# Optimization experiments

Hardware: AMD Instinct MI355X
Metric: run time of the kernel (lower is better)

The kernel has to match this reference:

```python
import jax, jax.numpy as jnp
import numpy as np

NUM_HEADS = 16
HEAD_DIM = 96          # dim=1536 / 16 heads
ROPE_HALF = HEAD_DIM // 2   # 48 rotary frequencies
FREQ_PER_AXIS = ROPE_HALF // 3  # 16 frequencies per 3D coordinate axis
ROPE_BASE = 10000.0


def _rope_sincos(coords):
    # coords: [B, T, 3] -> sin, cos: [B, T, ROPE_HALF]
    inv_freq = 1.0 / (ROPE_BASE ** (jnp.arange(FREQ_PER_AXIS, dtype=jnp.float32) / FREQ_PER_AXIS))
    # angles per axis: [B, T, 3, F] -> concat axes -> [B, T, 3*F]
    ang = coords[..., :, None] * inv_freq  # [B, T, 3, F]
    ang = ang.reshape(*coords.shape[:-1], ROPE_HALF)
    return jnp.sin(ang), jnp.cos(ang)


def _apply_rotary(x, sin, cos):
    # x: [B, H, T, D]; sin/cos: [B, T, D/2] broadcast over heads
    s = sin[:, None, :, :]
    c = cos[:, None, :, :]
    x1, x2 = x[..., :ROPE_HALF], x[..., ROPE_HALF:]
    return jnp.concatenate([x1 * c - x2 * s, x2 * c + x1 * s], axis=-1)


def setup_inputs() -> dict:
    key = jax.random.key(0)
    ks = jax.random.split(key, 8)
    B, Tq, Tk, D = 2, 1024, 2048, 1536
    std = 1.0 / np.sqrt(D)
    return {
        "x": jax.random.normal(ks[0], (B, Tq, D), jnp.float32),
        "memory": jax.random.normal(ks[1], (B, Tk, D), jnp.float32),
        "query_coords": jax.random.normal(ks[2], (B, Tq, 3), jnp.float32),
        "memory_coords": jax.random.normal(ks[3], (B, Tk, 3), jnp.float32),
        "Wq": jax.random.normal(ks[4], (D, D), jnp.float32) * std,
        "bq": jnp.zeros((D,), jnp.float32),
        "Wk": jax.random.normal(ks[5], (D, D), jnp.float32) * std,
        "bk": jnp.zeros((D,), jnp.float32),
        "Wv": jax.random.normal(ks[6], (D, D), jnp.float32) * std,
        "bv": jnp.zeros((D,), jnp.float32),
        "Wo": jax.random.normal(ks[7], (D, D), jnp.float32) * std,
        "bo": jnp.zeros((D,), jnp.float32),
    }


def reference(x, memory, query_coords, memory_coords, Wq, bq, Wk, bk, Wv, bv, Wo, bo):
    B, Tq, D = x.shape
    Tk = memory.shape[1]
    H, Hd = NUM_HEADS, HEAD_DIM

    # projections (nn.Linear: y = x @ W^T + b)
    q = (jnp.einsum('btd,ed->bte', x, Wq) + bq).reshape(B, Tq, H, Hd).transpose(0, 2, 1, 3)
    k = (jnp.einsum('btd,ed->bte', memory, Wk) + bk).reshape(B, Tk, H, Hd).transpose(0, 2, 1, 3)
    v = (jnp.einsum('btd,ed->bte', memory, Wv) + bv).reshape(B, Tk, H, Hd).transpose(0, 2, 1, 3)

    # 3D-coordinate RoPE (identity augmentation: shift=0, jitter=1, rescale=1)
    q_sin, q_cos = _rope_sincos(query_coords)
    k_sin, k_cos = _rope_sincos(memory_coords)
    q = _apply_rotary(q, q_sin, q_cos)
    k = _apply_rotary(k, k_sin, k_cos)

    # SDPA (standard scaling): softmax(q k^T / sqrt(Hd)) v
    scale = 1.0 / jnp.sqrt(jnp.asarray(Hd, jnp.float32))
    scores = jnp.einsum('bhqd,bhkd->bhqk', q, k) * scale
    attn = jax.nn.softmax(scores, axis=-1)
    out = jnp.einsum('bhqk,bhkd->bhqd', attn, v)  # [B, H, Tq, Hd]

    out = out.transpose(0, 2, 1, 3).reshape(B, Tq, D)
    return jnp.einsum('btd,ed->bte', out, Wo) + bo
```

## Files before the change

kernel.cpp:

```cpp
#include <hip/hip_runtime.h>
#include <math.h>

typedef _Float16 f16;
typedef __attribute__((ext_vector_type(4))) _Float16 f16x4;
typedef __attribute__((ext_vector_type(8))) _Float16 f16x8;
typedef __attribute__((ext_vector_type(4))) float f32x4;
typedef __attribute__((ext_vector_type(16))) float f32x16;

#define NB 2
#define NH 16
#define TQ 1024
#define TK 2048
#define DM 1536
#define HD 96
#define RH 48

__device__ __forceinline__ f32x4 mfma16(f16x8 a, f16x8 b, f32x4 c) {
    return __builtin_amdgcn_mfma_f32_16x16x32_f16(a, b, c, 0, 0, 0);
}

#define GLDS16(gptr, lptr) __builtin_amdgcn_global_load_lds( \
    (const __attribute__((address_space(1))) unsigned int*)(gptr), \
    (__attribute__((address_space(3))) unsigned int*)(lptr), 16, 0, 0)

__global__ void cvt_w4(const float4* __restrict__ W0, const float4* __restrict__ W1,
                       const float4* __restrict__ W2, const float4* __restrict__ W3,
                       f16x4* __restrict__ o0, f16x4* __restrict__ o1,
                       f16x4* __restrict__ o2, f16x4* __restrict__ o3, int n4) {
    int i = blockIdx.x * 256 + threadIdx.x;
    if (i >= n4) return;
    const float4* in = blockIdx.y == 0 ? W0 : blockIdx.y == 1 ? W1 : blockIdx.y == 2 ? W2 : W3;
    f16x4* out      = blockIdx.y == 0 ? o0 : blockIdx.y == 1 ? o1 : blockIdx.y == 2 ? o2 : o3;
    float4 v = in[i];
    f16x4 o;
    o[0] = (f16)v.x; o[1] = (f16)v.y; o[2] = (f16)v.z; o[3] = (f16)v.w;
    out[i] = o;
}

__global__ void cvt_xm(const float4* __restrict__ X, const float4* __restrict__ M,
                       f16x4* __restrict__ ox, f16x4* __restrict__ om, int nx4, int nm4) {
    int i = blockIdx.x * 256 + threadIdx.x;
    int n = blockIdx.y == 0 ? nx4 : nm4;
    if (i >= n) return;
    const float4* in = blockIdx.y == 0 ? X : M;
    f16x4* out = blockIdx.y == 0 ? ox : om;
    float4 v = in[i];
    f16x4 o;
    o[0] = (f16)v.x; o[1] = (f16)v.y; o[2] = (f16)v.z; o[3] = (f16)v.w;
    out[i] = o;
}

__global__ void rope_tab2(const float* __restrict__ cq, const float* __restrict__ cm,
                          float* __restrict__ sq, float* __restrict__ cqo,
                          float* __restrict__ sk, float* __restrict__ cko,
                          int nq, int nk) {
    int i = blockIdx.x * 256 + threadIdx.x;
    int n = blockIdx.y == 0 ? nq : nk;
    if (i >= n) return;
    const float* coords = blockIdx.y == 0 ? cq : cm;
    float* sinT = blockIdx.y == 0 ? sq : sk;
    float* cosT = blockIdx.y == 0 ? cqo : cko;
    int bt = i / 48, idx = i - bt * 48;
    int axis = idx >> 4, f = idx & 15;
    float inv = powf(10000.f, -(float)f * (1.f / 16.f));
    float ang = coords[bt * 3 + axis] * inv;
    sinT[i] = sinf(ang);
    cosT[i] = cosf(ang);
}

__global__ void rope_apply_k(f16* __restrict__ qk, const float* __restrict__ sinT,
                             const float* __restrict__ cosT, int T, int stride,
                             float scale, int n) {
    int i = blockIdx.x * 256 + threadIdx.x;
    if (i >= n) return;
    int p = i % 48;
    int rest = i / 48;
    int t = rest % T;
    int b = rest / (NH * T);
    long base = (long)rest * stride;
    float x1 = (float)qk[base + p];
    float x2 = (float)qk[base + p + RH];
    int ti = (b * T + t) * 48 + p;
    float s = sinT[ti], c = cosT[ti];
    qk[base + p]      = (f16)((x1 * c - x2 * s) * scale);
    qk[base + p + RH] = (f16)((x2 * c + x1 * s) * scale);
}

template <int CFG>
__global__ __launch_bounds__(CFG == 0 ? 512 : 256, CFG == 0 ? 1 : 2)
void gemmP(const f16* __restrict__ Aq, const f16* __restrict__ Akv,
           const f16* __restrict__ Wqp, const f16* __restrict__ Wkp, const f16* __restrict__ Wvp,
           const float* __restrict__ bqp, const float* __restrict__ bkp, const float* __restrict__ bvp,
           f16* __restrict__ outq, f16* __restrict__ outk, f16* __restrict__ outv,
           float* __restrict__ outo) {
    constexpr int BMx = CFG == 0 ? 256 : 128;
    constexpr int BNx = CFG == 0 ? 256 : 128;
    constexpr int TPB = CFG == 0 ? 512 : 256;
    constexpr int MI  = CFG == 0 ? 8 : 4;
    constexpr int NI  = 4;
    constexpr int ABUF = BMx * 64;
    constexpr int BUFSZ = (BMx + BNx) * 64;
    constexpr int NT = DM / 64;

    __shared__ f16 Buf[2][BUFSZ];

    const int tid = threadIdx.x, w = tid >> 6, lane = tid & 63;
    const int l15 = lane & 15, g = lane >> 4;

    int sel = 0, mt, nt;
    const f16* A; const f16* W; const float* bias;
    if constexpr (CFG == 0) {
        const int bid = blockIdx.x;
        const int wid = (bid & 7) * 30 + (bid >> 3);
        if (wid < 48)       { sel = 0; mt = wid / 6;        nt = wid - mt * 6;        A = Aq;  W = Wqp; bias = bqp; }
        else if (wid < 144) { sel = 1; int r = wid - 48;  mt = r / 6; nt = r - mt * 6; A = Akv; W = Wkp; bias = bkp; }
        else                { sel = 2; int r = wid - 144; mt = r / 6; nt = r - mt * 6; A = Akv; W = Wvp; bias = bvp; }
    } else {
        const int bid = blockIdx.x;
        const int wid = (bid & 7) * 24 + (bid >> 3);
        mt = wid / 12; nt = wid - mt * 12;
        A = Aq; W = Wqp; bias = bqp;
    }
    const int m0 = mt * BMx, n0 = nt * BNx;
    const int wm = (w & 1) * (MI * 16);
    const int wn = (w >> 1) * 64;

    int src[4];
#pragma unroll
    for (int r = 0; r < 4; r++) {
        int L = r * (TPB * 16) + tid * 16;
        int row = L >> 7, seg = (L >> 4) & 7;
        src[r] = row * DM + ((seg ^ (row & 7)) << 3);
    }
    const f16* Ag = A + (long)m0 * DM;
    const f16* Bg = W + (long)n0 * DM;

    int aoff[MI][2], boff[NI][2];
#pragma unroll
    for (int i = 0; i < MI; i++) {
        int row = wm + i * 16 + l15;
#pragma unroll
        for (int s = 0; s < 2; s++)
            aoff[i][s] = row * 64 + (((s * 4 + g) ^ (row & 7)) << 3);
    }
#pragma unroll
    for (int j = 0; j < NI; j++) {
        int row = wn + j * 16 + l15;
#pragma unroll
        for (int s = 0; s < 2; s++)
            boff[j][s] = ABUF + row * 64 + (((s * 4 + g) ^ (row & 7)) << 3);
    }

#define STG(bufp, kt) do { \
    _Pragma("unroll") for (int r_ = 0; r_ < 4; r_++) { \
        GLDS16(Ag + src[r_] + (kt) * 64, &Buf[bufp][r_ * (TPB * 8) + w * 512]); \
        GLDS16(Bg + src[r_] + (kt) * 64, &Buf[bufp][ABUF + r_ * (TPB * 8) + w * 512]); \
    } \
} while (0)

    f32x4 acc[MI][NI] = {};

#define COMPUTE(bufp) do { \
    f16x8 bf[NI][2]; \
    _Pragma("unroll") for (int j_ = 0; j_ < NI; j_++) \
        _Pragma("unroll") for (int s_ = 0; s_ < 2; s_++) \
            bf[j_][s_] = *(const f16x8*)&Buf[bufp][boff[j_][s_]]; \
    __builtin_amdgcn_s_setprio(1); \
    _Pragma("unroll") for (int i_ = 0; i_ < MI; i_++) { \
        f16x8 a0 = *(const f16x8*)&Buf[bufp][aoff[i_][0]]; \
        f16x8 a1 = *(const f16x8*)&Buf[bufp][aoff[i_][1]]; \
        _Pragma("unroll") for (int j_ = 0; j_ < NI; j_++) { \
            acc[i_][j_] = mfma16(a0, bf[j_][0], acc[i_][j_]); \
            acc[i_][j_] = mfma16(a1, bf[j_][1], acc[i_][j_]); \
        } \
    } \
    __builtin_amdgcn_s_setprio(0); \
} while (0)

    STG(0, 0);
#pragma unroll 1
    for (int t = 0; t < NT; t += 2) {
        STG(1, t + 1);
        asm volatile("s_waitcnt vmcnt(8)" ::: "memory");
        __builtin_amdgcn_s_barrier();
        __builtin_amdgcn_sched_barrier(0);
        COMPUTE(0);
        __builtin_amdgcn_sched_barrier(0);
        __builtin_amdgcn_s_barrier();
        if (t + 2 < NT) {
            STG(0, t + 2);
            asm volatile("s_waitcnt vmcnt(8)" ::: "memory");
        } else {
            asm volatile("s_waitcnt vmcnt(0)" ::: "memory");
        }
        __builtin_amdgcn_s_barrier();
        __builtin_amdgcn_sched_barrier(0);
        COMPUTE(1);
        __builtin_amdgcn_sched_barrier(0);
        __builtin_amdgcn_s_barrier();
    }
#undef STG
#undef COMPUTE

#pragma unroll
    for (int i = 0; i < MI; i++) {
#pragma unroll
        for (int j = 0; j < NI; j++) {
            const int n = n0 + wn + j * 16 + l15;
            const int mb = m0 + wm + i * 16 + g * 4;
            if constexpr (CFG == 1) {
#pragma unroll
                for (int r = 0; r < 4; r++)
                    outo[(long)(mb + r) * DM + n] = acc[i][j][r] + bias[n];
            } else {
                const int hh = n / HD, hd = n - hh * HD;
                if (sel == 0) {
#pragma unroll
                    for (int r = 0; r < 4; r++) {
                        int m = mb + r, bq = m >> 10, t = m & (TQ - 1);
                        outq[(((long)bq * NH + hh) * TQ + t) * 96 + hd] = (f16)(acc[i][j][r] + bias[n]);
                    }
                } else if (sel == 1) {
#pragma unroll
                    for (int r = 0; r < 4; r++) {
                        int m = mb + r, bq = m >> 11, t = m & (TK - 1);
                        outk[(((long)bq * NH + hh) * TK + t) * 128 + hd] = (f16)(acc[i][j][r] + bias[n]);
                    }
                } else {
                    int bq = mb >> 11, t = mb & (TK - 1);
                    f16x4 pk;
#pragma unroll
                    for (int r = 0; r < 4; r++) pk[r] = (f16)(acc[i][j][r] + bias[n]);
                    *(f16x4*)&outv[(((long)bq * NH + hh) * HD + hd) * TK + t] = pk;
                }
            }
        }
    }
}

__global__ __launch_bounds__(256, 2) void attn_fwd(
    const f16* __restrict__ Q, const f16* __restrict__ Kg,
    const f16* __restrict__ Vg, f16* __restrict__ O) {
    __shared__ f16 Kl[2][64 * 128];
    __shared__ f16 Vl[2][96 * 64];
    __shared__ f16 Pl[4][32 * 64];

    const int tid = threadIdx.x, w = tid >> 6, lane = tid & 63;
    const int q31 = lane & 31, hf = lane >> 5;
    const int half = w >> 1, u = w & 1;

    const int linear = blockIdx.x + (int)(gridDim.x * (blockIdx.y + gridDim.y * blockIdx.z));
    const int wid = (linear & 7) * 64 + (linear >> 3);
    const int qc = wid & 15, h = (wid >> 4) & 15, b = wid >> 8;

    const long kbase = (long)(b * NH + h) * TK * 128;
    const long vbase = (long)(b * NH + h) * HD * TK;
    const long qbase = (long)(b * NH + h) * TQ * 96;
    const int q0 = qc * 64 + u * 32;

    int ksrc[8], vsrc[6];
#pragma unroll
    for (int i = 0; i < 8; i++) {
        int L = (u * 8 + i) * 1024 + lane * 16;
        int r = L >> 8, s = (L >> 4) & 15;
        ksrc[i] = r * 128 + ((s ^ (r & 7)) << 3);
    }
#pragma unroll
    for (int i = 0; i < 6; i++) {
        int L = (u * 6 + i) * 1024 + lane * 16;
        int r = L >> 7, s = (L >> 4) & 7;
        vsrc[i] = r * TK + ((s ^ (r & 7)) << 3);
    }

    f16x8 qf[6];
#pragma unroll
    for (int s = 0; s < 6; s++)
        qf[s] = *(const f16x8*)&Q[qbase + (long)(q0 + q31) * 96 + hf * 8 + 16 * s];

    float mx = -3e38f, ls = 0.f;
    f32x16 acc[3] = {};

#define STAGE(c_) do { \
    const f16* kp_ = Kg + kbase + (long)(half * 16 + (c_)) * (64 * 128); \
    _Pragma("unroll") for (int i_ = 0; i_ < 8; i_++) \
        GLDS16(kp_ + ksrc[i_], &Kl[half][(u * 8 + i_) * 512]); \
    const f16* vp_ = Vg + vbase + (half * 16 + (c_)) * 64; \
    _Pragma("unroll") for (int i_ = 0; i_ < 6; i_++) \
        GLDS16(vp_ + vsrc[i_], &Vl[half][(u * 6 + i_) * 512]); \
} while (0)

    STAGE(0);

    for (int c = 0; c < 16; ++c) {
        __syncthreads();

        f32x16 st[2] = {};
#pragma unroll
        for (int kt = 0; kt < 2; kt++)
#pragma unroll
            for (int s = 0; s < 6; s++) {
                f16x8 kf = *(const f16x8*)&Kl[half][(kt * 32 + q31) * 128 +
                                                    (((hf + 2 * s) ^ (q31 & 7)) << 3)];
                st[kt] = __builtin_amdgcn_mfma_f32_32x32x16_f16(kf, qf[s], st[kt], 0, 0, 0);
            }

        float t16[16];
#pragma unroll
        for (int r = 0; r < 16; r++) t16[r] = fmaxf(st[0][r], st[1][r]);
#pragma unroll
        for (int o = 8; o >= 1; o >>= 1)
#pragma unroll
            for (int r = 0; r < o; r++) t16[r] = fmaxf(t16[r], t16[r + o]);
        float cm = fmaxf(t16[0], __shfl_xor(t16[0], 32));
        float mn = fmaxf(mx, cm);
        float corr = exp2f(mx - mn);
        mx = mn;
#pragma unroll
        for (int kt = 0; kt < 2; kt++)
#pragma unroll
            for (int r = 0; r < 16; r++) st[kt][r] = exp2f(st[kt][r] - mn);
        float s16[16];
#pragma unroll
        for (int r = 0; r < 16; r++) s16[r] = st[0][r] + st[1][r];
#pragma unroll
        for (int o = 8; o >= 1; o >>= 1)
#pragma unroll
            for (int r = 0; r < o; r++) s16[r] += s16[r + o];
        ls = ls * corr + s16[0];
#pragma unroll
        for (int dt = 0; dt < 3; dt++)
#pragma unroll
            for (int r = 0; r < 16; r++) acc[dt][r] *= corr;

#pragma unroll
        for (int kt = 0; kt < 2; kt++)
#pragma unroll
            for (int jq = 0; jq < 4; jq++) {
                f16x4 pk;
#pragma unroll
                for (int e = 0; e < 4; e++) pk[e] = (f16)st[kt][jq * 4 + e];
                int seg = kt * 4 + jq;
                *(f16x4*)&Pl[w][q31 * 64 + ((seg ^ (q31 & 7)) << 3) + hf * 4] = pk;
            }

#pragma unroll
        for (int ks = 0; ks < 4; ks++) {
            f16x8 pf = *(const f16x8*)&Pl[w][q31 * 64 + (((hf + 2 * ks) ^ (q31 & 7)) << 3)];
#pragma unroll
            for (int dt = 0; dt < 3; dt++) {
                f16x8 vf = *(const f16x8*)&Vl[half][(dt * 32 + q31) * 64 +
                                                    (((hf + 2 * ks) ^ (q31 & 7)) << 3)];
                acc[dt] = __builtin_amdgcn_mfma_f32_32x32x16_f16(vf, pf, acc[dt], 0, 0, 0);
            }
        }

        __syncthreads();
        if (c < 15) STAGE(c + 1);
    }

    ls += __shfl_xor(ls, 32);
    float* dump = (float*)&Kl[0][0] + u * (64 * 52);
    __syncthreads();
    if (half == 1) {
        float* dl = dump + lane * 52;
        dl[0] = mx; dl[1] = ls;
#pragma unroll
        for (int dt = 0; dt < 3; dt++)
#pragma unroll
            for (int r = 0; r < 16; r++) dl[2 + dt * 16 + r] = acc[dt][r];
    }
    __syncthreads();
    if (half == 0) {
        const float* dl = dump + lane * 52;
        float mb = dl[0], lsb = dl[1];
        float mf = fmaxf(mx, mb);
        float ca = exp2f(mx - mf), cb = exp2f(mb - mf);
        float inv = 1.f / (ls * ca + lsb * cb);
        const long orow = (long)(b * TQ + q0 + q31) * DM + h * 96;
#pragma unroll
        for (int dt = 0; dt < 3; dt++)
#pragma unroll
            for (int jq = 0; jq < 4; jq++) {
                f16x4 ov;
#pragma unroll
                for (int e = 0; e < 4; e++) {
                    int r = jq * 4 + e;
                    ov[e] = (f16)((acc[dt][r] * ca + dl[2 + dt * 16 + r] * cb) * inv);
                }
                *(f16x4*)&O[orow + dt * 32 + jq * 8 + hf * 4] = ov;
            }
    }
}

extern "C" void kernel_launch(void* const* d_in, const int* in_sizes, int n_in,
                              void* d_out, int out_size, void* d_ws, size_t ws_size,
                              hipStream_t stream) {
    const float* x   = (const float*)d_in[0];
    const float* mem = (const float*)d_in[1];
    const float* qc  = (const float*)d_in[2];
    const float* mc  = (const float*)d_in[3];
    const float* Wq  = (const float*)d_in[4];
    const float* bq  = (const float*)d_in[5];
    const float* Wk  = (const float*)d_in[6];
    const float* bk  = (const float*)d_in[7];
    const float* Wv  = (const float*)d_in[8];
    const float* bv  = (const float*)d_in[9];
    const float* Wo  = (const float*)d_in[10];
    const float* bo  = (const float*)d_in[11];
    float* out = (float*)d_out;

    const long nx  = (long)NB * TQ * DM;
    const long nm  = (long)NB * TK * DM;
    const long nw  = (long)DM * DM;
    const long nq  = (long)NB * NH * TQ * 96;
    const long nkp = (long)NB * NH * TK * 128;
    const long nvt = (long)NB * NH * HD * TK;

    char* ws = (char*)d_ws;
    size_t off = 0;
    auto alloc = [&](size_t bytes) { size_t o = off; off = (off + bytes + 255) & ~(size_t)255; return o; };
    f16* x16   = (f16*)(ws + alloc(nx * 2));
    f16* mem16 = (f16*)(ws + alloc(nm * 2));
    f16* wq16  = (f16*)(ws + alloc(nw * 2));
    f16* wk16  = (f16*)(ws + alloc(nw * 2));
    f16* wv16  = (f16*)(ws + alloc(nw * 2));
    f16* wo16  = (f16*)(ws + alloc(nw * 2));
    f16* q16   = (f16*)(ws + alloc(nq * 2));
    f16* k16p  = (f16*)(ws + alloc(nkp * 2));
    f16* vt16  = (f16*)(ws + alloc(nvt * 2));
    float* sinq = (float*)(ws + alloc((size_t)NB * TQ * 48 * 4));
    float* cosq = (float*)(ws + alloc((size_t)NB * TQ * 48 * 4));
    float* sink = (float*)(ws + alloc((size_t)NB * TK * 48 * 4));
    float* cosk = (float*)(ws + alloc((size_t)NB * TK * 48 * 4));
    f16* at16 = x16;

    cvt_w4<<<dim3((int)(nw / 4 / 256), 4), 256, 0, stream>>>(
        (const float4*)Wq, (const float4*)Wk, (const float4*)Wv, (const float4*)Wo,
        (f16x4*)wq16, (f16x4*)wk16, (f16x4*)wv16, (f16x4*)wo16, (int)(nw / 4));
    cvt_xm<<<dim3((int)(nm / 4 / 256), 2), 256, 0, stream>>>(
        (const float4*)x, (const float4*)mem, (f16x4*)x16, (f16x4*)mem16,
        (int)(nx / 4), (int)(nm / 4));

    rope_tab2<<<dim3((NB * TK * 48 + 255) / 256, 2), 256, 0, stream>>>(
        qc, mc, sinq, cosq, sink, cosk, NB * TQ * 48, NB * TK * 48);

    gemmP<0><<<240, 512, 0, stream>>>(
        x16, mem16, wq16, wk16, wv16, bq, bk, bv, q16, k16p, vt16, nullptr);

    const float qscale = 0.10206207261596577f * 1.4426950408889634f;
    rope_apply_k<<<(NB * NH * TQ * 48 + 255) / 256, 256, 0, stream>>>(
        q16, sinq, cosq, TQ, 96, qscale, NB * NH * TQ * 48);
    rope_apply_k<<<(NB * NH * TK * 48 + 255) / 256, 256, 0, stream>>>(
        k16p, sink, cosk, TK, 128, 1.0f, NB * NH * TK * 48);

    attn_fwd<<<dim3(16, 16, 2), 256, 0, stream>>>(q16, k16p, vt16, at16);

    gemmP<1><<<192, 256, 0, stream>>>(
        at16, nullptr, wo16, nullptr, nullptr, bo, nullptr, nullptr,
        nullptr, nullptr, nullptr, out);
}
```

Measured before the change: 158.7 us.

## Split GEMM k-step into four quadrant phases to cut registers and allow two blocks

Replaces the per-k-tile compute, which loaded all B fragments and then streamed A, with four quadrant phases. Each phase loads only half the A or B fragments and issues its MFMAs between barriers, ping-ponging the fragments. This lowers live fragment registers so the 512-thread projection GEMM can target two blocks per CU, and it adds intra-iteration barriers for wave interleaving. The risks are extra barrier synchronisation, possible register spills under the tighter bound, and an LDS budget that may not fit two blocks.

After: 160.2 us. Within noise of the previous version (+1.0%).

```diff
diff --git a/kernel.cpp b/kernel.cpp
--- a/kernel.cpp
+++ b/kernel.cpp
@@ -87,7 +87,7 @@
 }
 
 template <int CFG>
-__global__ __launch_bounds__(CFG == 0 ? 512 : 256, CFG == 0 ? 1 : 2)
+__global__ __launch_bounds__(CFG == 0 ? 512 : 256, 2)
 void gemmP(const f16* __restrict__ Aq, const f16* __restrict__ Akv,
            const f16* __restrict__ Wqp, const f16* __restrict__ Wkp, const f16* __restrict__ Wvp,
            const float* __restrict__ bqp, const float* __restrict__ bkp, const float* __restrict__ bvp,
@@ -98,6 +98,7 @@
     constexpr int TPB = CFG == 0 ? 512 : 256;
     constexpr int MI  = CFG == 0 ? 8 : 4;
     constexpr int NI  = 4;
+    constexpr int MH  = MI / 2;
     constexpr int ABUF = BMx * 64;
     constexpr int BUFSZ = (BMx + BNx) * 64;
     constexpr int NT = DM / 64;
@@ -160,47 +161,84 @@
 
     f32x4 acc[MI][NI] = {};
 
-#define COMPUTE(bufp) do { \
-    f16x8 bf[NI][2]; \
-    _Pragma("unroll") for (int j_ = 0; j_ < NI; j_++) \
-        _Pragma("unroll") for (int s_ = 0; s_ < 2; s_++) \
-            bf[j_][s_] = *(const f16x8*)&Buf[bufp][boff[j_][s_]]; \
-    __builtin_amdgcn_s_setprio(1); \
-    _Pragma("unroll") for (int i_ = 0; i_ < MI; i_++) { \
-        f16x8 a0 = *(const f16x8*)&Buf[bufp][aoff[i_][0]]; \
-        f16x8 a1 = *(const f16x8*)&Buf[bufp][aoff[i_][1]]; \
-        _Pragma("unroll") for (int j_ = 0; j_ < NI; j_++) { \
-            acc[i_][j_] = mfma16(a0, bf[j_][0], acc[i_][j_]); \
-            acc[i_][j_] = mfma16(a1, bf[j_][1], acc[i_][j_]); \
-        } \
-    } \
-    __builtin_amdgcn_s_setprio(0); \
-} while (0)
-
     STG(0, 0);
 #pragma unroll 1
-    for (int t = 0; t < NT; t += 2) {
-        STG(1, t + 1);
-        asm volatile("s_waitcnt vmcnt(8)" ::: "memory");
-        __builtin_amdgcn_s_barrier();
-        __builtin_amdgcn_sched_barrier(0);
-        COMPUTE(0);
-        __builtin_amdgcn_sched_barrier(0);
-        __builtin_amdgcn_s_barrier();
-        if (t + 2 < NT) {
-            STG(0, t + 2);
+    for (int t = 0; t < NT; ++t) {
+        const int bi = t & 1;
+        if (t + 1 < NT) {
+            STG(bi ^ 1, t + 1);
             asm volatile("s_waitcnt vmcnt(8)" ::: "memory");
         } else {
             asm volatile("s_waitcnt vmcnt(0)" ::: "memory");
         }
         __builtin_amdgcn_s_barrier();
         __builtin_amdgcn_sched_barrier(0);
-        COMPUTE(1);
-        __builtin_amdgcn_sched_barrier(0);
+        const f16* bp = &Buf[bi][0];
+
+        f16x8 af[MH][2], bfL[2][2], bfH[2][2];
+#pragma unroll
+        for (int i = 0; i < MH; i++)
+#pragma unroll
+            for (int s = 0; s < 2; s++) af[i][s] = *(const f16x8*)&bp[aoff[i][s]];
+#pragma unroll
+        for (int j = 0; j < 2; j++)
+#pragma unroll
+            for (int s = 0; s < 2; s++) bfL[j][s] = *(const f16x8*)&bp[boff[j][s]];
+        __builtin_amdgcn_sched_barrier(0);
+        __builtin_amdgcn_s_setprio(1);
+#pragma unroll
+        for (int i = 0; i < MH; i++)
+#pragma unroll
+            for (int j = 0; j < 2; j++)
+#pragma unroll
+                for (int s = 0; s < 2; s++)
+                    acc[i][j] = mfma16(af[i][s], bfL[j][s], acc[i][j]);
+        __builtin_amdgcn_s_setprio(0);
         __builtin_amdgcn_s_barrier();
+        __builtin_amdgcn_sched_barrier(0);
+#pragma unroll
+        for (int j = 0; j < 2; j++)
+#pragma unroll
+            for (int s = 0; s < 2; s++) bfH[j][s] = *(const f16x8*)&bp[boff[2 + j][s]];
+        __builtin_amdgcn_sched_barrier(0);
+        __builtin_amdgcn_s_setprio(1);
+#pragma unroll
+        for (int i = 0; i < MH; i++)
+#pragma unroll
+            for (int j = 0; j < 2; j++)
+#pragma unroll
+                for (int s = 0; s < 2; s++)
+                    acc[i][2 + j] = mfma16(af[i][s], bfH[j][s], acc[i][2 + j]);
+        __builtin_amdgcn_s_setprio(0);
+        __builtin_amdgcn_s_barrier();
+        __builtin_amdgcn_sched_barrier(0);
+#pragma unroll
+        for (int i = 0; i < MH; i++)
+#pragma unroll
+            for (int s = 0; s < 2; s++) af[i][s] = *(const f16x8*)&bp[aoff[MH + i][s]];
+        __builtin_amdgcn_sched_barrier(0);
+        __builtin_amdgcn_s_setprio(1);
+#pragma unroll
+        for (int i = 0; i < MH; i++)
+#pragma unroll
+            for (int j = 0; j < 2; j++)
+#pragma unroll
+                for (int s = 0; s < 2; s++)
+                    acc[MH + i][2 + j] = mfma16(af[i][s], bfH[j][s], acc[MH + i][2 + j]);
+        __builtin_amdgcn_s_setprio(0);
+        __builtin_amdgcn_s_barrier();
+        __builtin_amdgcn_sched_barrier(0);
+        __builtin_amdgcn_s_setprio(1);
+#pragma unroll
+        for (int i = 0; i < MH; i++)
+#pragma unroll
+            for (int j = 0; j < 2; j++)
+#pragma unroll
+                for (int s = 0; s < 2; s++)
+                    acc[MH + i][j] = mfma16(af[i][s], bfL[j][s], acc[MH + i][j]);
+        __builtin_amdgcn_s_setprio(0);
     }
 #undef STG
-#undef COMPUTE
 
 #pragma unroll
     for (int i = 0; i < MI; i++) {
```

## Switch projection GEMM to 32x32x16 MFMA with software-pipelined LDS reads

Applied to the files above, without the earlier changes.

Rewrites the projection GEMM inner loop to use 32x32x16 MFMA tiles instead of 16x16x32, which halves the fragment loads per FLOP. LDS fragment reads for the next k-slice are interleaved with the MFMAs of the current one, and the main loop now processes one k-tile per iteration with a single double-buffer swap. It also raises the minimum-blocks hint for the 512-thread config to 2, which pressures registers. The aim is higher MFMA throughput and fewer LDS reads, at the cost of larger accumulators that might spill.

New measurement: 164.9 us, median of 2. +3.9%, slower.

```diff
diff --git a/kernel.cpp b/kernel.cpp
--- a/kernel.cpp
+++ b/kernel.cpp
@@ -87,7 +87,7 @@
 }
 
 template <int CFG>
-__global__ __launch_bounds__(CFG == 0 ? 512 : 256, CFG == 0 ? 1 : 2)
+__global__ __launch_bounds__(CFG == 0 ? 512 : 256, 2)
 void gemmP(const f16* __restrict__ Aq, const f16* __restrict__ Akv,
            const f16* __restrict__ Wqp, const f16* __restrict__ Wkp, const f16* __restrict__ Wvp,
            const float* __restrict__ bqp, const float* __restrict__ bkp, const float* __restrict__ bvp,
@@ -96,8 +96,7 @@
     constexpr int BMx = CFG == 0 ? 256 : 128;
     constexpr int BNx = CFG == 0 ? 256 : 128;
     constexpr int TPB = CFG == 0 ? 512 : 256;
-    constexpr int MI  = CFG == 0 ? 8 : 4;
-    constexpr int NI  = 4;
+    constexpr int MT  = CFG == 0 ? 4 : 2;
     constexpr int ABUF = BMx * 64;
     constexpr int BUFSZ = (BMx + BNx) * 64;
     constexpr int NT = DM / 64;
@@ -105,7 +104,7 @@
     __shared__ f16 Buf[2][BUFSZ];
 
     const int tid = threadIdx.x, w = tid >> 6, lane = tid & 63;
-    const int l15 = lane & 15, g = lane >> 4;
+    const int q31 = lane & 31, hf = lane >> 5;
 
     int sel = 0, mt, nt;
     const f16* A; const f16* W; const float* bias;
@@ -122,7 +121,7 @@
         A = Aq; W = Wqp; bias = bqp;
     }
     const int m0 = mt * BMx, n0 = nt * BNx;
-    const int wm = (w & 1) * (MI * 16);
+    const int wm = (w & 1) * (MT * 32);
     const int wn = (w >> 1) * 64;
 
     int src[4];
@@ -135,20 +134,20 @@
     const f16* Ag = A + (long)m0 * DM;
     const f16* Bg = W + (long)n0 * DM;
 
-    int aoff[MI][2], boff[NI][2];
-#pragma unroll
-    for (int i = 0; i < MI; i++) {
-        int row = wm + i * 16 + l15;
-#pragma unroll
-        for (int s = 0; s < 2; s++)
-            aoff[i][s] = row * 64 + (((s * 4 + g) ^ (row & 7)) << 3);
-    }
-#pragma unroll
-    for (int j = 0; j < NI; j++) {
-        int row = wn + j * 16 + l15;
-#pragma unroll
-        for (int s = 0; s < 2; s++)
-            boff[j][s] = ABUF + row * 64 + (((s * 4 + g) ^ (row & 7)) << 3);
+    int aoff[MT][4], boff[2][4];
+#pragma unroll
+    for (int i = 0; i < MT; i++) {
+        int row = wm + i * 32 + q31;
+#pragma unroll
+        for (int ks = 0; ks < 4; ks++)
+            aoff[i][ks] = row * 64 + (((ks * 2 + hf) ^ (row & 7)) << 3);
+    }
+#pragma unroll
+    for (int j = 0; j < 2; j++) {
+        int row = wn + j * 32 + q31;
+#pragma unroll
+        for (int ks = 0; ks < 4; ks++)
+            boff[j][ks] = ABUF + row * 64 + (((ks * 2 + hf) ^ (row & 7)) << 3);
     }
 
 #define STG(bufp, kt) do { \
@@ -158,80 +157,92 @@
     } \
 } while (0)
 
-    f32x4 acc[MI][NI] = {};
-
-#define COMPUTE(bufp) do { \
-    f16x8 bf[NI][2]; \
-    _Pragma("unroll") for (int j_ = 0; j_ < NI; j_++) \
-        _Pragma("unroll") for (int s_ = 0; s_ < 2; s_++) \
-            bf[j_][s_] = *(const f16x8*)&Buf[bufp][boff[j_][s_]]; \
+#define RD(aset, bset, ks) do { \
+    _Pragma("unroll") for (int i_ = 0; i_ < MT; i_++) \
+        aset[i_] = *(const f16x8*)&bp[aoff[i_][ks]]; \
+    _Pragma("unroll") for (int j_ = 0; j_ < 2; j_++) \
+        bset[j_] = *(const f16x8*)&bp[boff[j_][ks]]; \
+} while (0)
+
+#define MM(aset, bset) do { \
     __builtin_amdgcn_s_setprio(1); \
-    _Pragma("unroll") for (int i_ = 0; i_ < MI; i_++) { \
-        f16x8 a0 = *(const f16x8*)&Buf[bufp][aoff[i_][0]]; \
-        f16x8 a1 = *(const f16x8*)&Buf[bufp][aoff[i_][1]]; \
-        _Pragma("unroll") for (int j_ = 0; j_ < NI; j_++) { \
-            acc[i_][j_] = mfma16(a0, bf[j_][0], acc[i_][j_]); \
-            acc[i_][j_] = mfma16(a1, bf[j_][1], acc[i_][j_]); \
-        } \
-    } \
+    _Pragma("unroll") for (int i_ = 0; i_ < MT; i_++) \
+        _Pragma("unroll") for (int j_ = 0; j_ < 2; j_++) \
+            acc[i_][j_] = __builtin_amdgcn_mfma_f32_32x32x16_f16(aset[i_], bset[j_], acc[i_][j_], 0, 0, 0); \
     __builtin_amdgcn_s_setprio(0); \
 } while (0)
 
+    f32x16 acc[MT][2] = {};
+
     STG(0, 0);
 #pragma unroll 1
-    for (int t = 0; t < NT; t += 2) {
-        STG(1, t + 1);
-        asm volatile("s_waitcnt vmcnt(8)" ::: "memory");
-        __builtin_amdgcn_s_barrier();
-        __builtin_amdgcn_sched_barrier(0);
-        COMPUTE(0);
-        __builtin_amdgcn_sched_barrier(0);
-        __builtin_amdgcn_s_barrier();
-        if (t + 2 < NT) {
-            STG(0, t + 2);
+    for (int t = 0; t < NT; ++t) {
+        const int bi = t & 1;
+        if (t + 1 < NT) {
+            STG(bi ^ 1, t + 1);
             asm volatile("s_waitcnt vmcnt(8)" ::: "memory");
         } else {
             asm volatile("s_waitcnt vmcnt(0)" ::: "memory");
         }
         __builtin_amdgcn_s_barrier();
         __builtin_amdgcn_sched_barrier(0);
-        COMPUTE(1);
+        const f16* bp = &Buf[bi][0];
+
+        f16x8 fa0[MT], fb0[2], fa1[MT], fb1[2];
+        RD(fa0, fb0, 0);
+        RD(fa1, fb1, 1);
+        MM(fa0, fb0);
+        RD(fa0, fb0, 2);
+        MM(fa1, fb1);
+        RD(fa1, fb1, 3);
+        MM(fa0, fb0);
+        asm volatile("s_waitcnt lgkmcnt(0)" ::: "memory");
         __builtin_amdgcn_sched_barrier(0);
         __builtin_amdgcn_s_barrier();
+        MM(fa1, fb1);
     }
 #undef STG
-#undef COMPUTE
-
-#pragma unroll
-    for (int i = 0; i < MI; i++) {
-#pragma unroll
-        for (int j = 0; j < NI; j++) {
-            const int n = n0 + wn + j * 16 + l15;
-            const int mb = m0 + wm + i * 16 + g * 4;
+#undef RD
+#undef MM
+
+#pragma unroll
+    for (int i = 0; i < MT; i++) {
+#pragma unroll
+        for (int j = 0; j < 2; j++) {
+            const int n = n0 + wn + j * 32 + q31;
+            const float bn = bias[n];
             if constexpr (CFG == 1) {
 #pragma unroll
-                for (int r = 0; r < 4; r++)
-                    outo[(long)(mb + r) * DM + n] = acc[i][j][r] + bias[n];
+                for (int r = 0; r < 16; r++) {
+                    int m = m0 + wm + i * 32 + (r & 3) + 8 * (r >> 2) + 4 * hf;
+                    outo[(long)m * DM + n] = acc[i][j][r] + bn;
+                }
             } else {
                 const int hh = n / HD, hd = n - hh * HD;
                 if (sel == 0) {
 #pragma unroll
-                    for (int r = 0; r < 4; r++) {
-                        int m = mb + r, bq = m >> 10, t = m & (TQ - 1);
-                        outq[(((long)bq * NH + hh) * TQ + t) * 96 + hd] = (f16)(acc[i][j][r] + bias[n]);
+                    for (int r = 0; r < 16; r++) {
+                        int m = m0 + wm + i * 32 + (r & 3) + 8 * (r >> 2) + 4 * hf;
+                        int bq = m >> 10, t = m & (TQ - 1);
+                        outq[(((long)bq * NH + hh) * TQ + t) * 96 + hd] = (f16)(acc[i][j][r] + bn);
                     }
                 } else if (sel == 1) {
 #pragma unroll
-                    for (int r = 0; r < 4; r++) {
-                        int m = mb + r, bq = m >> 11, t = m & (TK - 1);
-                        outk[(((long)bq * NH + hh) * TK + t) * 128 + hd] = (f16)(acc[i][j][r] + bias[n]);
+                    for (int r = 0; r < 16; r++) {
+                        int m = m0 + wm + i * 32 + (r & 3) + 8 * (r >> 2) + 4 * hf;
+                        int bq = m >> 11, t = m & (TK - 1);
+                        outk[(((long)bq * NH + hh) * TK + t) * 128 + hd] = (f16)(acc[i][j][r] + bn);
                     }
                 } else {
-                    int bq = mb >> 11, t = mb & (TK - 1);
-                    f16x4 pk;
-#pragma unroll
-                    for (int r = 0; r < 4; r++) pk[r] = (f16)(acc[i][j][r] + bias[n]);
-                    *(f16x4*)&outv[(((long)bq * NH + hh) * HD + hd) * TK + t] = pk;
+#pragma unroll
+                    for (int g = 0; g < 4; g++) {
+                        int mb = m0 + wm + i * 32 + 8 * g + 4 * hf;
+                        int bq = mb >> 11, t = mb & (TK - 1);
+                        f16x4 pk;
+#pragma unroll
+                        for (int e = 0; e < 4; e++) pk[e] = (f16)(acc[i][j][4 * g + e] + bn);
+                        *(f16x4*)&outv[(((long)bq * NH + hh) * HD + hd) * TK + t] = pk;
+                    }
                 }
             }
         }
```

## Fuse Q rotary into attention, vectorize K rotary, merge conversion kernels

Applied to the files above, without the earlier changes.

Three changes. Q-side RoPE and softmax scaling now run inside the attention kernel on the Q fragments right after they are loaded, so the separate Q rope pass over global memory goes away. The K rope kernel is rewritten to handle 4 elements per thread with vector loads. The weight and activation fp32-to-fp16 conversions are merged into one launch. Together these cut kernel launches and memory traffic, at the cost of extra sin/cos loads in attention and idle blocks in the merged conversion grid, which is sized for the largest tensor.

Result: no change. 155.8 us (-1.8%).

```diff
diff --git a/kernel.cpp b/kernel.cpp
--- a/kernel.cpp
+++ b/kernel.cpp
@@ -23,27 +23,19 @@
     (const __attribute__((address_space(1))) unsigned int*)(gptr), \
     (__attribute__((address_space(3))) unsigned int*)(lptr), 16, 0, 0)
 
-__global__ void cvt_w4(const float4* __restrict__ W0, const float4* __restrict__ W1,
-                       const float4* __restrict__ W2, const float4* __restrict__ W3,
-                       f16x4* __restrict__ o0, f16x4* __restrict__ o1,
-                       f16x4* __restrict__ o2, f16x4* __restrict__ o3, int n4) {
+__global__ void cvt6(const float4* __restrict__ Wq, const float4* __restrict__ Wk,
+                     const float4* __restrict__ Wv, const float4* __restrict__ Wo,
+                     const float4* __restrict__ X,  const float4* __restrict__ M,
+                     f16x4* __restrict__ oq, f16x4* __restrict__ ok,
+                     f16x4* __restrict__ ov, f16x4* __restrict__ oo,
+                     f16x4* __restrict__ ox, f16x4* __restrict__ om,
+                     int nw4, int nx4, int nm4) {
     int i = blockIdx.x * 256 + threadIdx.x;
-    if (i >= n4) return;
-    const float4* in = blockIdx.y == 0 ? W0 : blockIdx.y == 1 ? W1 : blockIdx.y == 2 ? W2 : W3;
-    f16x4* out      = blockIdx.y == 0 ? o0 : blockIdx.y == 1 ? o1 : blockIdx.y == 2 ? o2 : o3;
-    float4 v = in[i];
-    f16x4 o;
-    o[0] = (f16)v.x; o[1] = (f16)v.y; o[2] = (f16)v.z; o[3] = (f16)v.w;
-    out[i] = o;
-}
-
-__global__ void cvt_xm(const float4* __restrict__ X, const float4* __restrict__ M,
-                       f16x4* __restrict__ ox, f16x4* __restrict__ om, int nx4, int nm4) {
-    int i = blockIdx.x * 256 + threadIdx.x;
-    int n = blockIdx.y == 0 ? nx4 : nm4;
+    const int y = blockIdx.y;
+    const int n = (y < 4) ? nw4 : (y == 4 ? nx4 : nm4);
     if (i >= n) return;
-    const float4* in = blockIdx.y == 0 ? X : M;
-    f16x4* out = blockIdx.y == 0 ? ox : om;
+    const float4* in = y == 0 ? Wq : y == 1 ? Wk : y == 2 ? Wv : y == 3 ? Wo : y == 4 ? X : M;
+    f16x4* out      = y == 0 ? oq : y == 1 ? ok : y == 2 ? ov : y == 3 ? oo : y == 4 ? ox : om;
     float4 v = in[i];
     f16x4 o;
     o[0] = (f16)v.x; o[1] = (f16)v.y; o[2] = (f16)v.z; o[3] = (f16)v.w;
@@ -68,22 +60,29 @@
     cosT[i] = cosf(ang);
 }
 
-__global__ void rope_apply_k(f16* __restrict__ qk, const float* __restrict__ sinT,
-                             const float* __restrict__ cosT, int T, int stride,
-                             float scale, int n) {
+__global__ void ropek4(f16* __restrict__ qk, const float* __restrict__ sinT,
+                       const float* __restrict__ cosT, int n) {
     int i = blockIdx.x * 256 + threadIdx.x;
     if (i >= n) return;
-    int p = i % 48;
-    int rest = i / 48;
-    int t = rest % T;
-    int b = rest / (NH * T);
-    long base = (long)rest * stride;
-    float x1 = (float)qk[base + p];
-    float x2 = (float)qk[base + p + RH];
-    int ti = (b * T + t) * 48 + p;
-    float s = sinT[ti], c = cosT[ti];
-    qk[base + p]      = (f16)((x1 * c - x2 * s) * scale);
-    qk[base + p + RH] = (f16)((x2 * c + x1 * s) * scale);
+    int j = i % 12, row = i / 12;
+    int p0 = j * 4;
+    int t = row & (TK - 1);
+    int b = row / (NH * TK);
+    long base = (long)row * 128;
+    float4 sv = *(const float4*)&sinT[((long)b * TK + t) * 48 + p0];
+    float4 cv = *(const float4*)&cosT[((long)b * TK + t) * 48 + p0];
+    f16x4 x1 = *(const f16x4*)&qk[base + p0];
+    f16x4 x2 = *(const f16x4*)&qk[base + p0 + RH];
+    f16x4 o1, o2;
+    float s[4] = {sv.x, sv.y, sv.z, sv.w}, c[4] = {cv.x, cv.y, cv.z, cv.w};
+#pragma unroll
+    for (int e = 0; e < 4; e++) {
+        float a = (float)x1[e], bb = (float)x2[e];
+        o1[e] = (f16)(a * c[e] - bb * s[e]);
+        o2[e] = (f16)(bb * c[e] + a * s[e]);
+    }
+    *(f16x4*)&qk[base + p0] = o1;
+    *(f16x4*)&qk[base + p0 + RH] = o2;
 }
 
 template <int CFG>
@@ -240,7 +239,8 @@
 
 __global__ __launch_bounds__(256, 2) void attn_fwd(
     const f16* __restrict__ Q, const f16* __restrict__ Kg,
-    const f16* __restrict__ Vg, f16* __restrict__ O) {
+    const f16* __restrict__ Vg, const float* __restrict__ sinq,
+    const float* __restrict__ cosq, f16* __restrict__ O) {
     __shared__ f16 Kl[2][64 * 128];
     __shared__ f16 Vl[2][96 * 64];
     __shared__ f16 Pl[4][32 * 64];
@@ -276,6 +276,25 @@
 #pragma unroll
     for (int s = 0; s < 6; s++)
         qf[s] = *(const f16x8*)&Q[qbase + (long)(q0 + q31) * 96 + hf * 8 + 16 * s];
+    {
+        const float QS = 0.10206207261596577f * 1.4426950408889634f;
+        const long tb = ((long)b * TQ + q0 + q31) * 48 + hf * 8;
+#pragma unroll
+        for (int s = 0; s < 3; s++) {
+            float4 s0 = *(const float4*)&sinq[tb + 16 * s];
+            float4 s1 = *(const float4*)&sinq[tb + 16 * s + 4];
+            float4 c0 = *(const float4*)&cosq[tb + 16 * s];
+            float4 c1 = *(const float4*)&cosq[tb + 16 * s + 4];
+            float sv[8] = {s0.x, s0.y, s0.z, s0.w, s1.x, s1.y, s1.z, s1.w};
+            float cv[8] = {c0.x, c0.y, c0.z, c0.w, c1.x, c1.y, c1.z, c1.w};
+#pragma unroll
+            for (int e = 0; e < 8; e++) {
+                float x1 = (float)qf[s][e], x2 = (float)qf[s + 3][e];
+                qf[s][e]     = (f16)((x1 * cv[e] - x2 * sv[e]) * QS);
+                qf[s + 3][e] = (f16)((x2 * cv[e] + x1 * sv[e]) * QS);
+            }
+        }
+    }
 
     float mx = -3e38f, ls = 0.f;
     f32x16 acc[3] = {};
@@ -434,12 +453,12 @@
     float* cosk = (float*)(ws + alloc((size_t)NB * TK * 48 * 4));
     f16* at16 = x16;
 
-    cvt_w4<<<dim3((int)(nw / 4 / 256), 4), 256, 0, stream>>>(
+    cvt6<<<dim3((int)(nm / 4 / 256), 6), 256, 0, stream>>>(
         (const float4*)Wq, (const float4*)Wk, (const float4*)Wv, (const float4*)Wo,
-        (f16x4*)wq16, (f16x4*)wk16, (f16x4*)wv16, (f16x4*)wo16, (int)(nw / 4));
-    cvt_xm<<<dim3((int)(nm / 4 / 256), 2), 256, 0, stream>>>(
-        (const float4*)x, (const float4*)mem, (f16x4*)x16, (f16x4*)mem16,
-        (int)(nx / 4), (int)(nm / 4));
+        (const float4*)x, (const float4*)mem,
+        (f16x4*)wq16, (f16x4*)wk16, (f16x4*)wv16, (f16x4*)wo16,
+        (f16x4*)x16, (f16x4*)mem16,
+        (int)(nw / 4), (int)(nx / 4), (int)(nm / 4));
 
     rope_tab2<<<dim3((NB * TK * 48 + 255) / 256, 2), 256, 0, stream>>>(
         qc, mc, sinq, cosq, sink, cosk, NB * TQ * 48, NB * TK * 48);
@@ -447,13 +466,10 @@
     gemmP<0><<<240, 512, 0, stream>>>(
         x16, mem16, wq16, wk16, wv16, bq, bk, bv, q16, k16p, vt16, nullptr);
 
-    const float qscale = 0.10206207261596577f * 1.4426950408889634f;
-    rope_apply_k<<<(NB * NH * TQ * 48 + 255) / 256, 256, 0, stream>>>(
-        q16, sinq, cosq, TQ, 96, qscale, NB * NH * TQ * 48);
-    rope_apply_k<<<(NB * NH * TK * 48 + 255) / 256, 256, 0, stream>>>(
-        k16p, sink, cosk, TK, 128, 1.0f, NB * NH * TK * 48);
-
-    attn_fwd<<<dim3(16, 16, 2), 256, 0, stream>>>(q16, k16p, vt16, at16);
+    ropek4<<<(NB * NH * TK * 12 + 255) / 256, 256, 0, stream>>>(
+        k16p, sink, cosk, NB * NH * TK * 12);
+
+    attn_fwd<<<dim3(16, 16, 2), 256, 0, stream>>>(q16, k16p, vt16, sinq, cosq, at16);
 
     gemmP<1><<<192, 256, 0, stream>>>(
         at16, nullptr, wo16, nullptr, nullptr, bo, nullptr, nullptr,
```
